# Kernel optimization log

Measured on AMD Instinct MI355X. Metric: run time of the kernel, lower is better.

Reference implementation:

```python
import jax, jax.numpy as jnp
import numpy as np

P = 14            # pooled resolution
S = 2             # sampling ratio (samples per bin per axis)
SCALE = 0.0625    # spatial scale (1/16)
TRANS_STD = 0.1   # offset std multiplier
C = 256           # feature channels
FC = 1024         # offset-mlp hidden dim
N_ROIS = 192
B, H, W = 2, 128, 128


def deform_ps_roi_pool(x, rois, offset):
    """Modulated deformable (PS)RoI pooling core (DCNv2 dcn_v2_psroi, group_size=1).
    x: [B,C,H,W], rois: [N,5] (b,x1,y1,x2,y2), offset: [N,2,P,P] -> [N,C,P,P]."""
    Bn, Cn, Hn, Wn = x.shape
    xt = jnp.transpose(x, (0, 2, 3, 1))  # [B,H,W,C]
    b = rois[:, 0].astype(jnp.int32)
    x1, y1, x2, y2 = rois[:, 1], rois[:, 2], rois[:, 3], rois[:, 4]
    sw = jnp.round(x1) * SCALE - 0.5
    sh = jnp.round(y1) * SCALE - 0.5
    ew = (jnp.round(x2) + 1.0) * SCALE - 0.5
    eh = (jnp.round(y2) + 1.0) * SCALE - 0.5
    rw = jnp.maximum(ew - sw, 0.1)  # [N]
    rh = jnp.maximum(eh - sh, 0.1)
    bw, bh = rw / P, rh / P
    subw = (bw / S)[:, None, None, None, None]
    subh = (bh / S)[:, None, None, None, None]
    phg, pwg = jnp.meshgrid(jnp.arange(P), jnp.arange(P), indexing="ij")  # [P,P]
    tx = offset[:, 0] * TRANS_STD  # [N,P,P]
    ty = offset[:, 1] * TRANS_STD
    wstart = pwg[None] * bw[:, None, None] + sw[:, None, None] + tx * rw[:, None, None]
    hstart = phg[None] * bh[:, None, None] + sh[:, None, None] + ty * rh[:, None, None]
    ihg, iwg = jnp.meshgrid(jnp.arange(S), jnp.arange(S), indexing="ij")  # [S,S]
    w = wstart[..., None, None] + iwg * subw  # [N,P,P,S,S]
    h = hstart[..., None, None] + ihg * subh
    valid = (w >= -0.5) & (w <= Wn - 0.5) & (h >= -0.5) & (h <= Hn - 0.5)
    wc = jnp.clip(w, 0.0, Wn - 1.0)
    hc = jnp.clip(h, 0.0, Hn - 1.0)
    x0 = jnp.floor(wc).astype(jnp.int32)
    y0 = jnp.floor(hc).astype(jnp.int32)
    x1i = jnp.minimum(x0 + 1, Wn - 1)
    y1i = jnp.minimum(y0 + 1, Hn - 1)
    lx = (wc - x0)[..., None]
    ly = (hc - y0)[..., None]
    bb = b[:, None, None, None, None]
    g = lambda yy, xx: xt[bb, yy, xx]  # [N,P,P,S,S,C] bilinear corner gather
    val = ((1 - ly) * (1 - lx)) * g(y0, x0) + ((1 - ly) * lx) * g(y0, x1i) \
        + (ly * (1 - lx)) * g(y1i, x0) + (ly * lx) * g(y1i, x1i)
    val = val * valid[..., None]
    cnt = valid.sum(axis=(3, 4)).astype(x.dtype)  # [N,P,P]
    out = val.sum(axis=(3, 4)) / jnp.maximum(cnt, 1.0)[..., None]  # [N,P,P,C]
    return jnp.transpose(out, (0, 3, 1, 2))  # [N,C,P,P]


def setup_inputs() -> dict:
    key = jax.random.key(0)
    ks = jax.random.split(key, 12)
    x = jax.random.normal(ks[0], (B, C, H, W), dtype=jnp.float32)
    img = W / SCALE  # 2048 px image
    bx1 = jax.random.uniform(ks[1], (N_ROIS,), minval=0.0, maxval=img - 500.0)
    by1 = jax.random.uniform(ks[2], (N_ROIS,), minval=0.0, maxval=img - 500.0)
    bw_ = jax.random.uniform(ks[3], (N_ROIS,), minval=64.0, maxval=480.0)
    bh_ = jax.random.uniform(ks[4], (N_ROIS,), minval=64.0, maxval=480.0)
    bid = jnp.sort(jax.random.randint(ks[5], (N_ROIS,), 0, B)).astype(jnp.float32)
    rois = jnp.stack([bid, bx1, by1, jnp.minimum(bx1 + bw_, img - 1.0),
                      jnp.minimum(by1 + bh_, img - 1.0)], axis=1)
    D = C * P * P
    w1 = jax.random.normal(ks[6], (D, FC), dtype=jnp.float32) * 0.01
    b1 = jnp.zeros((FC,), jnp.float32)
    w2 = jax.random.normal(ks[7], (FC, FC), dtype=jnp.float32) * 0.01
    b2 = jnp.zeros((FC,), jnp.float32)
    w3 = jax.random.normal(ks[8], (FC, 3 * P * P), dtype=jnp.float32) * 0.01
    b3 = jnp.zeros((3 * P * P,), jnp.float32)
    return {"x": x, "rois": rois, "w1": w1, "b1": b1, "w2": w2, "b2": b2, "w3": w3, "b3": b3}


def reference(x, rois, w1, b1, w2, b2, w3, b3):
    n = rois.shape[0]
    # pass 1: zero-offset pooling to feed the offset/mask MLP
    zero_off = jnp.zeros((n, 2, P, P), x.dtype)
    base = deform_ps_roi_pool(x, rois, zero_off)  # [N,C,P,P]
    f = base.reshape(n, -1)
    f = jax.nn.relu(f @ w1 + b1)
    f = jax.nn.relu(f @ w2 + b2)
    om = f @ w3 + b3  # [N, 3*P*P]
    off = om[:, : 2 * P * P].reshape(n, 2, P, P)
    mask = jax.nn.sigmoid(om[:, 2 * P * P:]).reshape(n, 1, P, P)
    # pass 2: deformable pooling at learned offsets, modulated by mask
    return deform_ps_roi_pool(x, rois, off) * mask
```

## Files before the change

kernel.cpp:

```cpp
#include <hip/hip_runtime.h>

#define PBIN 14
#define SSAMP 2
#define SCALE_F 0.0625f
#define TRANS_STD 0.1f
#define CCH 256
#define FCDIM 1024
#define NROIS 192
#define HH 128
#define WW 128
#define PP (PBIN*PBIN)
#define KDIM (CCH*PP)

typedef __bf16 bf16x8 __attribute__((ext_vector_type(8)));
typedef float  f32x4  __attribute__((ext_vector_type(4)));
typedef unsigned u32x4 __attribute__((ext_vector_type(4)));
typedef unsigned u32x2 __attribute__((ext_vector_type(2)));

__device__ __forceinline__ unsigned short f2bf(float f) {
  unsigned u = __builtin_bit_cast(unsigned, f);
  u += 0x7FFFu + ((u >> 16) & 1u);
  return (unsigned short)(u >> 16);
}
__device__ __forceinline__ unsigned pk2(float lo, float hi) {
  unsigned ulo = __builtin_bit_cast(unsigned, lo) + 0x8000u;
  unsigned uhi = __builtin_bit_cast(unsigned, hi) + 0x8000u;
  return __builtin_amdgcn_perm(uhi, ulo, 0x07060302u);
}
__device__ __forceinline__ float bf_lo(unsigned u) {
  return __builtin_bit_cast(float, u << 16);
}
__device__ __forceinline__ float bf_hi(unsigned u) {
  return __builtin_bit_cast(float, u & 0xFFFF0000u);
}
__device__ __forceinline__ float bf_u16(unsigned short v) {
  return __builtin_bit_cast(float, (unsigned)v << 16);
}

__global__ __launch_bounds__(256) void transpose_x_kernel(
    const float* __restrict__ x, unsigned* __restrict__ xt)
{
  __shared__ float tile[32][33];
  int tx = threadIdx.x, ty = threadIdx.y;
  int hw0 = blockIdx.x * 32;
  int c0  = blockIdx.y * 32;
  int b   = blockIdx.z;
  const float* xb = x + (size_t)b * CCH * HH * WW;
  unsigned* xtb   = xt + (size_t)b * (HH*WW) * (CCH/2);
#pragma unroll
  for (int k = 0; k < 4; ++k)
    tile[ty + k*8][tx] = xb[(size_t)(c0 + ty + k*8) * (HH*WW) + hw0 + tx];
  __syncthreads();
  int l  = ty*32 + tx;
  int cp = l & 15;
  int hr = l >> 4;
#pragma unroll
  for (int k = 0; k < 2; ++k) {
    int row = hr + k*16;
    unsigned pkd = pk2(tile[2*cp][row], tile[2*cp+1][row]);
    xtb[(size_t)(hw0 + row) * (CCH/2) + (c0>>1) + cp] = pkd;
  }
}

template<int MODE>
__global__ __launch_bounds__(256) void pool_kernel(
    const unsigned* __restrict__ xt, const float* __restrict__ rois,
    const unsigned short* __restrict__ p3, const float* __restrict__ b3, int S3,
    void* __restrict__ outp)
{
  __shared__ float lds[4][256];
  const int t = threadIdx.x;
  const int wv = t >> 6, lane = t & 63;
  const int n  = blockIdx.x;
  const int p0 = blockIdx.y * 4;
  const int p  = p0 + wv;
  const int ph = p / PBIN, pw = p % PBIN;

  float rb = rois[n*5 + 0];
  float x1 = rois[n*5 + 1], y1 = rois[n*5 + 2];
  float x2 = rois[n*5 + 3], y2 = rois[n*5 + 4];
  int b = (int)rb;
  float sw = rintf(x1) * SCALE_F - 0.5f;
  float sh = rintf(y1) * SCALE_F - 0.5f;
  float ew = (rintf(x2) + 1.0f) * SCALE_F - 0.5f;
  float eh = (rintf(y2) + 1.0f) * SCALE_F - 0.5f;
  float rw = fmaxf(ew - sw, 0.1f);
  float rh = fmaxf(eh - sh, 0.1f);
  float bw = rw / PBIN, bh = rh / PBIN;
  float subw = bw / SSAMP, subh = bh / SSAMP;

  float tx = 0.f, ty = 0.f, mval = 1.f;
  if (MODE == 1) {
    float a0 = b3[p], a1 = b3[PP + p], a2 = b3[2*PP + p];
#pragma unroll 4
    for (int s = 0; s < S3; ++s) {
      size_t ba = ((size_t)s*NROIS + n) * (3*PP);
      a0 += bf_u16(p3[ba + p]);
      a1 += bf_u16(p3[ba + PP + p]);
      a2 += bf_u16(p3[ba + 2*PP + p]);
    }
    tx = a0 * TRANS_STD;
    ty = a1 * TRANS_STD;
    mval = 1.0f / (1.0f + expf(-a2));
  }
  float wstart = pw * bw + sw + tx * rw;
  float hstart = ph * bh + sh + ty * rh;

  int offs[16];
  float wts[16];
  float cnt = 0.f;
  int base_b = b * (HH*WW);
#pragma unroll
  for (int ih = 0; ih < SSAMP; ++ih) {
#pragma unroll
    for (int iw = 0; iw < SSAMP; ++iw) {
      float wv_ = wstart + iw * subw;
      float hv_ = hstart + ih * subh;
      float validf = (wv_ >= -0.5f && wv_ <= WW - 0.5f &&
                      hv_ >= -0.5f && hv_ <= HH - 0.5f) ? 1.f : 0.f;
      cnt += validf;
      float wc = fminf(fmaxf(wv_, 0.f), WW - 1.0f);
      float hc = fminf(fmaxf(hv_, 0.f), HH - 1.0f);
      int x0 = (int)floorf(wc), y0 = (int)floorf(hc);
      int x1i = min(x0 + 1, WW - 1), y1i = min(y0 + 1, HH - 1);
      float lx = wc - (float)x0, ly = hc - (float)y0;
      int s4 = (ih*2 + iw) * 4;
      offs[s4+0] = (base_b + y0 *WW + x0 ) * (CCH/2);
      offs[s4+1] = (base_b + y0 *WW + x1i) * (CCH/2);
      offs[s4+2] = (base_b + y1i*WW + x0 ) * (CCH/2);
      offs[s4+3] = (base_b + y1i*WW + x1i) * (CCH/2);
      wts[s4+0] = validf * (1.f-ly)*(1.f-lx);
      wts[s4+1] = validf * (1.f-ly)*lx;
      wts[s4+2] = validf * ly*(1.f-lx);
      wts[s4+3] = validf * ly*lx;
    }
  }
  float inv = 1.0f / fmaxf(cnt, 1.0f);
  if (MODE == 1) inv *= mval;

  const int cl = lane * 4;
  f32x4 acc = {0.f, 0.f, 0.f, 0.f};
#pragma unroll
  for (int s = 0; s < 16; ++s) {
    u32x2 v = *(const u32x2*)&xt[offs[s] + lane*2];
    acc[0] += wts[s] * bf_lo(v[0]);
    acc[1] += wts[s] * bf_hi(v[0]);
    acc[2] += wts[s] * bf_lo(v[1]);
    acc[3] += wts[s] * bf_hi(v[1]);
  }
  acc *= inv;

  if (MODE == 0) {
    unsigned short* bout = (unsigned short*)outp;
    u32x2 pkd = { pk2(acc[0], acc[1]), pk2(acc[2], acc[3]) };
    *(u32x2*)&bout[(size_t)n*KDIM + p*CCH + cl] = pkd;
  } else {
    *(f32x4*)&lds[wv][cl] = acc;
    __syncthreads();
    float* fout = (float*)outp;
    int c = t;
    f32x4 o = { lds[0][c], lds[1][c], lds[2][c], lds[3][c] };
    *(f32x4*)&fout[(size_t)n*KDIM + (size_t)c*PP + p0] = o;
  }
}

template<int PERM, int SWZ>
__global__ __launch_bounds__(512, 4) void gemm_splitk(
    const unsigned* __restrict__ A, int ldAu,
    const float* __restrict__ Bm, int N, int ldB,
    unsigned short* __restrict__ partial, int NB, int S, int chunks)
{
  __shared__ __align__(16) unsigned lds_a[192*20];
  __shared__ __align__(16) unsigned lds_b[128*18];

  int t   = threadIdx.x;
  int bid = blockIdx.x;
  int s, nblk;
  if (SWZ) {
    int xcd = bid & 7;
    nblk    = (bid >> 3) & 7;
    s       = xcd * (S >> 3) + (bid >> 6);
  } else {
    nblk = bid % NB;
    s    = bid / NB;
  }
  int n0 = nblk * 128;
  int q = chunks / S, r = chunks % S;
  int myc = q + (s < r ? 1 : 0);
  int c0 = s*q + (s < r ? s : r);
  int k0 = c0 * 32;

  int wv = t >> 6, lane = t & 63;
  int wm = wv & 3, wn = wv >> 2;
  int m0w = wm * 48;
  int n0w = wn * 64;
  int lrow = lane & 15, lg = lane >> 4;

  f32x4 acc[3][4];
#pragma unroll
  for (int i = 0; i < 3; ++i)
#pragma unroll
    for (int j = 0; j < 4; ++j) acc[i][j] = {0.f,0.f,0.f,0.f};

  u32x2 areg[3];
  float bv[8];
  const int am  = t >> 3;
  const int akp = (t & 7) * 2;
  const int bn  = t & 127;
  const int bk8 = (t >> 7) * 8;

  auto load_tile = [&](int it) {
    int kg = k0 + it*32;
#pragma unroll
    for (int i = 0; i < 3; ++i) {
      int m = am + i*64;
      areg[i] = *(const u32x2*)&A[(size_t)m*ldAu + (kg>>1) + akp];
    }
    int gn = n0 + bn;
    bool okn = (gn < N);
#pragma unroll
    for (int i = 0; i < 8; ++i) {
      int rr = kg + bk8 + i;
      size_t srow = PERM ? ((size_t)(rr & 255)*PP + (rr >> 8)) : (size_t)rr;
      bv[i] = okn ? Bm[srow*ldB + gn] : 0.f;
    }
  };

  load_tile(0);
  for (int it = 0; it < myc; ++it) {
    __syncthreads();
#pragma unroll
    for (int i = 0; i < 3; ++i) {
      int m = am + i*64;
      *(u32x2*)&lds_a[m*20 + akp] = areg[i];
    }
    {
      u32x2 w01 = { pk2(bv[0], bv[1]), pk2(bv[2], bv[3]) };
      u32x2 w23 = { pk2(bv[4], bv[5]), pk2(bv[6], bv[7]) };
      *(u32x2*)&lds_b[bn*18 + (bk8>>1)]     = w01;
      *(u32x2*)&lds_b[bn*18 + (bk8>>1) + 2] = w23;
    }
    __syncthreads();
    if (it + 1 < myc) load_tile(it + 1);

    bf16x8 af[3];
#pragma unroll
    for (int mf = 0; mf < 3; ++mf) {
      u32x4 ra = *(const u32x4*)&lds_a[(m0w + mf*16 + lrow)*20 + lg*4];
      af[mf] = __builtin_bit_cast(bf16x8, ra);
    }
    bf16x8 bfrag[4];
#pragma unroll
    for (int nf = 0; nf < 4; ++nf) {
      int col = n0w + nf*16 + lrow;
      u32x2 r0 = *(const u32x2*)&lds_b[col*18 + lg*4];
      u32x2 r1 = *(const u32x2*)&lds_b[col*18 + lg*4 + 2];
      u32x4 ub = { r0[0], r0[1], r1[0], r1[1] };
      bfrag[nf] = __builtin_bit_cast(bf16x8, ub);
    }
#pragma unroll
    for (int nf = 0; nf < 4; ++nf)
#pragma unroll
      for (int mf = 0; mf < 3; ++mf)
        acc[mf][nf] = __builtin_amdgcn_mfma_f32_16x16x32_bf16(af[mf], bfrag[nf], acc[mf][nf], 0, 0, 0);
  }

#pragma unroll
  for (int mf = 0; mf < 3; ++mf) {
#pragma unroll
    for (int nf = 0; nf < 4; ++nf) {
      int gcol = n0 + n0w + nf*16 + lrow;
      if (gcol < N) {
#pragma unroll
        for (int rr = 0; rr < 4; ++rr) {
          int m = m0w + mf*16 + lg*4 + rr;
          partial[((size_t)s*NROIS + m)*N + gcol] = f2bf(acc[mf][nf][rr]);
        }
      }
    }
  }
}

__global__ __launch_bounds__(256) void reduce_kernel(
    const unsigned short* __restrict__ partial, const float* __restrict__ bias,
    unsigned short* __restrict__ outp, int N, int S)
{
  int nn = (blockIdx.x*256 + threadIdx.x) * 4;
  int m  = blockIdx.y;
  if (nn >= N) return;
  f32x4 a = *(const f32x4*)&bias[nn];
  size_t stride = (size_t)NROIS * N;
  const unsigned short* p = &partial[(size_t)m*N + nn];
#pragma unroll 4
  for (int s = 0; s < S; ++s) {
    u32x2 v = *(const u32x2*)&p[(size_t)s*stride];
    a[0] += bf_lo(v[0]); a[1] += bf_hi(v[0]);
    a[2] += bf_lo(v[1]); a[3] += bf_hi(v[1]);
  }
  a[0] = fmaxf(a[0], 0.f); a[1] = fmaxf(a[1], 0.f);
  a[2] = fmaxf(a[2], 0.f); a[3] = fmaxf(a[3], 0.f);
  u32x2 pkd = { pk2(a[0], a[1]), pk2(a[2], a[3]) };
  *(u32x2*)&outp[(size_t)m*N + nn] = pkd;
}

extern "C" void kernel_launch(void* const* d_in, const int* in_sizes, int n_in,
                              void* d_out, int out_size, void* d_ws, size_t ws_size,
                              hipStream_t stream)
{
  const float* x    = (const float*)d_in[0];
  const float* rois = (const float*)d_in[1];
  const float* w1   = (const float*)d_in[2];
  const float* b1   = (const float*)d_in[3];
  const float* w2   = (const float*)d_in[4];
  const float* b2   = (const float*)d_in[5];
  const float* w3   = (const float*)d_in[6];
  const float* b3   = (const float*)d_in[7];

  char* ws = (char*)d_ws;
  size_t off = 0;
  unsigned* xt = (unsigned*)(ws + off);               off += (size_t)2*(HH*WW)*(CCH/2)*4;
  unsigned short* base = (unsigned short*)(ws + off); off += (size_t)NROIS*KDIM*2;
  unsigned short* f1 = (unsigned short*)(ws + off);   off += (size_t)NROIS*FCDIM*2;
  unsigned short* f2 = (unsigned short*)(ws + off);   off += (size_t)NROIS*FCDIM*2;
  const int S1 = 64, S2 = 32, S3 = 16;
  unsigned short* partial1 = (unsigned short*)(ws + off); off += (size_t)S1*NROIS*FCDIM*2;
  unsigned short* partial2 = (unsigned short*)(ws + off); off += (size_t)S2*NROIS*FCDIM*2;
  unsigned short* partial3 = (unsigned short*)(ws + off); off += (size_t)S3*NROIS*(3*PP)*2;
  (void)ws_size;

  transpose_x_kernel<<<dim3(512, 8, 2), dim3(32, 8), 0, stream>>>(x, xt);
  pool_kernel<0><<<dim3(NROIS, PP/4), 256, 0, stream>>>(xt, rois, nullptr, nullptr, 0, base);
  gemm_splitk<1,1><<<8*S1, 512, 0, stream>>>((const unsigned*)base, KDIM/2, w1, FCDIM, FCDIM, partial1, 8, S1, KDIM/32);
  reduce_kernel<<<dim3(1, NROIS), 256, 0, stream>>>(partial1, b1, f1, FCDIM, S1);
  gemm_splitk<0,1><<<8*S2, 512, 0, stream>>>((const unsigned*)f1, FCDIM/2, w2, FCDIM, FCDIM, partial2, 8, S2, FCDIM/32);
  reduce_kernel<<<dim3(1, NROIS), 256, 0, stream>>>(partial2, b2, f2, FCDIM, S2);
  gemm_splitk<0,0><<<5*S3, 512, 0, stream>>>((const unsigned*)f2, FCDIM/2, w3, 3*PP, 3*PP, partial3, 5, S3, FCDIM/32);
  pool_kernel<1><<<dim3(NROIS, PP/4), 256, 0, stream>>>(xt, rois, partial3, b3, S3, d_out);
}
```

Measured before the change: 171.6 us.

## Vectorize weight loads in split-K GEMM, widen pool gathers, separate offset reduction

The split-K GEMM now loads the fp32 weight matrix as 4-wide vectors across columns and packs pairs of k rows into bf16 in LDS, in place of scalar strided loads. This is meant to cut the instruction and transaction cost of streaming the large w1 matrix. The pool kernel now gives each half-wave 8 of the 16 bilinear corner samples, each lane doing a 16-byte gather, and merges the halves with a cross-half shuffle. The third-layer split-K partials are summed once by a new reduce kernel instead of in every pool block. This adds a launch and an fp32 buffer in the workspace, and the new LDS write pattern for B may cause bank conflicts.

```diff
diff --git a/kernel.cpp b/kernel.cpp
--- a/kernel.cpp
+++ b/kernel.cpp
@@ -65,8 +65,7 @@
 template<int MODE>
 __global__ __launch_bounds__(256) void pool_kernel(
     const unsigned* __restrict__ xt, const float* __restrict__ rois,
-    const unsigned short* __restrict__ p3, const float* __restrict__ b3, int S3,
-    void* __restrict__ outp)
+    const float* __restrict__ om, void* __restrict__ outp)
 {
   __shared__ float lds[4][256];
   const int t = threadIdx.x;
@@ -91,17 +90,10 @@
 
   float tx = 0.f, ty = 0.f, mval = 1.f;
   if (MODE == 1) {
-    float a0 = b3[p], a1 = b3[PP + p], a2 = b3[2*PP + p];
-#pragma unroll 4
-    for (int s = 0; s < S3; ++s) {
-      size_t ba = ((size_t)s*NROIS + n) * (3*PP);
-      a0 += bf_u16(p3[ba + p]);
-      a1 += bf_u16(p3[ba + PP + p]);
-      a2 += bf_u16(p3[ba + 2*PP + p]);
-    }
-    tx = a0 * TRANS_STD;
-    ty = a1 * TRANS_STD;
-    mval = 1.0f / (1.0f + expf(-a2));
+    const float* omr = om + (size_t)n * (3*PP);
+    tx = omr[p] * TRANS_STD;
+    ty = omr[PP + p] * TRANS_STD;
+    mval = 1.0f / (1.0f + expf(-omr[2*PP + p]));
   }
   float wstart = pw * bw + sw + tx * rw;
   float hstart = ph * bh + sh + ty * rh;
@@ -138,24 +130,34 @@
   float inv = 1.0f / fmaxf(cnt, 1.0f);
   if (MODE == 1) inv *= mval;
 
-  const int cl = lane * 4;
-  f32x4 acc = {0.f, 0.f, 0.f, 0.f};
-#pragma unroll
-  for (int s = 0; s < 16; ++s) {
-    u32x2 v = *(const u32x2*)&xt[offs[s] + lane*2];
-    acc[0] += wts[s] * bf_lo(v[0]);
-    acc[1] += wts[s] * bf_hi(v[0]);
-    acc[2] += wts[s] * bf_lo(v[1]);
-    acc[3] += wts[s] * bf_hi(v[1]);
-  }
-  acc *= inv;
+  const int h = lane >> 5;
+  const int j = lane & 31;
+  f32x4 a0 = {0.f,0.f,0.f,0.f}, a1 = {0.f,0.f,0.f,0.f};
+#pragma unroll
+  for (int q = 0; q < 8; ++q) {
+    int   off = h ? offs[q+8] : offs[q];
+    float w   = h ? wts[q+8]  : wts[q];
+    u32x4 v = *(const u32x4*)&xt[off + 4*j];
+    a0[0] += w * bf_lo(v[0]); a0[1] += w * bf_hi(v[0]);
+    a0[2] += w * bf_lo(v[1]); a0[3] += w * bf_hi(v[1]);
+    a1[0] += w * bf_lo(v[2]); a1[1] += w * bf_hi(v[2]);
+    a1[2] += w * bf_lo(v[3]); a1[3] += w * bf_hi(v[3]);
+  }
+#pragma unroll
+  for (int e = 0; e < 4; ++e) {
+    a0[e] += __shfl_xor(a0[e], 32, 64);
+    a1[e] += __shfl_xor(a1[e], 32, 64);
+  }
+  f32x4 av = h ? a1 : a0;
+  av *= inv;
+  const int ch = 8*j + 4*h;
 
   if (MODE == 0) {
     unsigned short* bout = (unsigned short*)outp;
-    u32x2 pkd = { pk2(acc[0], acc[1]), pk2(acc[2], acc[3]) };
-    *(u32x2*)&bout[(size_t)n*KDIM + p*CCH + cl] = pkd;
+    u32x2 pkd = { pk2(av[0], av[1]), pk2(av[2], av[3]) };
+    *(u32x2*)&bout[(size_t)n*KDIM + p*CCH + ch] = pkd;
   } else {
-    *(f32x4*)&lds[wv][cl] = acc;
+    *(f32x4*)&lds[wv][ch] = av;
     __syncthreads();
     float* fout = (float*)outp;
     int c = t;
@@ -203,11 +205,11 @@
     for (int j = 0; j < 4; ++j) acc[i][j] = {0.f,0.f,0.f,0.f};
 
   u32x2 areg[3];
-  float bv[8];
+  f32x4 bva, bvb;
   const int am  = t >> 3;
   const int akp = (t & 7) * 2;
-  const int bn  = t & 127;
-  const int bk8 = (t >> 7) * 8;
+  const int nq  = t & 31;
+  const int ku  = t >> 5;
 
   auto load_tile = [&](int it) {
     int kg = k0 + it*32;
@@ -216,13 +218,19 @@
       int m = am + i*64;
       areg[i] = *(const u32x2*)&A[(size_t)m*ldAu + (kg>>1) + akp];
     }
-    int gn = n0 + bn;
-    bool okn = (gn < N);
-#pragma unroll
-    for (int i = 0; i < 8; ++i) {
-      int rr = kg + bk8 + i;
-      size_t srow = PERM ? ((size_t)(rr & 255)*PP + (rr >> 8)) : (size_t)rr;
-      bv[i] = okn ? Bm[srow*ldB + gn] : 0.f;
+    int ka = kg + 2*ku, kb = ka + 1;
+    size_t sra = PERM ? ((size_t)(ka & 255)*PP + (ka >> 8)) : (size_t)ka;
+    size_t srb = PERM ? ((size_t)(kb & 255)*PP + (kb >> 8)) : (size_t)kb;
+    int gn = n0 + nq*4;
+    if (gn + 3 < N) {
+      bva = *(const f32x4*)&Bm[sra*ldB + gn];
+      bvb = *(const f32x4*)&Bm[srb*ldB + gn];
+    } else {
+#pragma unroll
+      for (int e = 0; e < 4; ++e) {
+        bva[e] = (gn + e < N) ? Bm[sra*ldB + gn + e] : 0.f;
+        bvb[e] = (gn + e < N) ? Bm[srb*ldB + gn + e] : 0.f;
+      }
     }
   };
 
@@ -234,12 +242,9 @@
       int m = am + i*64;
       *(u32x2*)&lds_a[m*20 + akp] = areg[i];
     }
-    {
-      u32x2 w01 = { pk2(bv[0], bv[1]), pk2(bv[2], bv[3]) };
-      u32x2 w23 = { pk2(bv[4], bv[5]), pk2(bv[6], bv[7]) };
-      *(u32x2*)&lds_b[bn*18 + (bk8>>1)]     = w01;
-      *(u32x2*)&lds_b[bn*18 + (bk8>>1) + 2] = w23;
-    }
+#pragma unroll
+    for (int jj = 0; jj < 4; ++jj)
+      lds_b[(nq*4 + jj)*18 + ku] = pk2(bva[jj], bvb[jj]);
     __syncthreads();
     if (it + 1 < myc) load_tile(it + 1);
 
@@ -303,6 +308,20 @@
   *(u32x2*)&outp[(size_t)m*N + nn] = pkd;
 }
 
+__global__ __launch_bounds__(640) void reduce3_kernel(
+    const unsigned short* __restrict__ p3, const float* __restrict__ b3,
+    float* __restrict__ om, int S)
+{
+  int d = threadIdx.x;
+  int nn = blockIdx.x;
+  if (d >= 3*PP) return;
+  float a = b3[d];
+#pragma unroll 4
+  for (int s = 0; s < S; ++s)
+    a += bf_u16(p3[((size_t)s*NROIS + nn)*(3*PP) + d]);
+  om[(size_t)nn*(3*PP) + d] = a;
+}
+
 extern "C" void kernel_launch(void* const* d_in, const int* in_sizes, int n_in,
                               void* d_out, int out_size, void* d_ws, size_t ws_size,
                               hipStream_t stream)
@@ -322,6 +341,7 @@
   unsigned short* base = (unsigned short*)(ws + off); off += (size_t)NROIS*KDIM*2;
   unsigned short* f1 = (unsigned short*)(ws + off);   off += (size_t)NROIS*FCDIM*2;
   unsigned short* f2 = (unsigned short*)(ws + off);   off += (size_t)NROIS*FCDIM*2;
+  float* om = (float*)(ws + off);                     off += (size_t)NROIS*(3*PP)*4;
   const int S1 = 64, S2 = 32, S3 = 16;
   unsigned short* partial1 = (unsigned short*)(ws + off); off += (size_t)S1*NROIS*FCDIM*2;
   unsigned short* partial2 = (unsigned short*)(ws + off); off += (size_t)S2*NROIS*FCDIM*2;
@@ -329,11 +349,12 @@
   (void)ws_size;
 
   transpose_x_kernel<<<dim3(512, 8, 2), dim3(32, 8), 0, stream>>>(x, xt);
-  pool_kernel<0><<<dim3(NROIS, PP/4), 256, 0, stream>>>(xt, rois, nullptr, nullptr, 0, base);
+  pool_kernel<0><<<dim3(NROIS, PP/4), 256, 0, stream>>>(xt, rois, nullptr, base);
   gemm_splitk<1,1><<<8*S1, 512, 0, stream>>>((const unsigned*)base, KDIM/2, w1, FCDIM, FCDIM, partial1, 8, S1, KDIM/32);
   reduce_kernel<<<dim3(1, NROIS), 256, 0, stream>>>(partial1, b1, f1, FCDIM, S1);
   gemm_splitk<0,1><<<8*S2, 512, 0, stream>>>((const unsigned*)f1, FCDIM/2, w2, FCDIM, FCDIM, partial2, 8, S2, FCDIM/32);
   reduce_kernel<<<dim3(1, NROIS), 256, 0, stream>>>(partial2, b2, f2, FCDIM, S2);
   gemm_splitk<0,0><<<5*S3, 512, 0, stream>>>((const unsigned*)f2, FCDIM/2, w3, 3*PP, 3*PP, partial3, 5, S3, FCDIM/32);
-  pool_kernel<1><<<dim3(NROIS, PP/4), 256, 0, stream>>>(xt, rois, partial3, b3, S3, d_out);
-}
+  reduce3_kernel<<<NROIS, 640, 0, stream>>>(partial3, b3, om, S3);
+  pool_kernel<1><<<dim3(NROIS, PP/4), 256, 0, stream>>>(xt, rois, om, d_out);
+}
```

Result: slower. 231.6 us (+35.0%).
